# Kernel optimization log

Hardware: AMD Instinct MI355X
Metric: run time of the kernel (lower is better)

The kernel has to match this reference:

```python
import jax, jax.numpy as jnp
import numpy as np

FEAT_STRIDE = 16
SCORE_THRESH = 0.7
DIST_THRESH = 16.0
MAX_OUT = 50
B = 2048
IMG_W = 65536


def setup_inputs() -> dict:
    key = jax.random.key(0)
    k1, k2, k3 = jax.random.split(key, 3)
    fw = IMG_W // FEAT_STRIDE
    pred_cls_logit = jax.random.normal(k1, (B, fw), dtype=jnp.float32)
    pred_delta = jax.random.normal(k2, (B, fw, 2), dtype=jnp.float32)
    # realistic image widths in [0.5, 1.0] * img_width
    real_images_width = jax.random.uniform(k3, (B,), jnp.float32, 0.5, 1.0) * IMG_W
    return {
        "pred_cls_logit": pred_cls_logit,
        "pred_delta": pred_delta,
        "img_width": IMG_W,
        "real_images_width": real_images_width,
    }


def _nms_one(positions, scores):
    # positions: [N, 2], scores: [N]. Greedy 1D NMS, fixed MAX_OUT iterations.
    centers = positions.mean(axis=1)                      # [N]
    alive0 = scores >= SCORE_THRESH                       # score-threshold filter

    def step(alive, _):
        masked = jnp.where(alive, scores, -1e30)
        i = jnp.argmax(masked)                            # highest remaining score
        has = jnp.any(alive)
        f = has.astype(jnp.float32)                       # 1.0 if a box was picked
        p = positions[i] * f
        s = scores[i] * f
        # suppress everything within DIST_THRESH of picked center (incl. itself)
        new_alive = alive & (jnp.abs(centers - centers[i]) > DIST_THRESH)
        return new_alive, (p, s, f)

    _, (P, S, F) = jax.lax.scan(step, alive0, None, length=MAX_OUT)
    # pad_to_fixed_size: append validity flag column, zero-padded rows
    nms_positions = jnp.concatenate([P, F[:, None]], axis=1)   # [MAX_OUT, 3]
    nms_scores = jnp.concatenate([S[:, None], F[:, None]], axis=1)  # [MAX_OUT, 2]
    return nms_positions, nms_scores


def reference(pred_cls_logit, pred_delta, img_width, real_images_width):
    feat_width = img_width // FEAT_STRIDE
    interval_center = (jnp.arange(feat_width, dtype=jnp.float32) + 0.5) * FEAT_STRIDE
    # [B, feat_width, 2]
    pos = pred_delta * FEAT_STRIDE + interval_center[None, :, None]
    scores = jax.nn.sigmoid(pred_cls_logit)               # [B, feat_width]
    max_width = real_images_width[:, None, None] - 1.0
    pos = jnp.where(pos < 0.0, 0.0, pos)
    pos = jnp.where(pos > max_width, max_width, pos)

    nms_positions, nms_scores = jax.vmap(_nms_one)(pos, scores)

    nms_center = nms_positions[..., :2].mean(axis=2)      # [B, MAX_OUT]
    x_interval_num = jnp.floor(nms_center / FEAT_STRIDE).astype(jnp.int32)
    valid = nms_positions[..., 2] == 1.0
    idx = jnp.where(valid, x_interval_num, feat_width)    # out-of-range -> dropped
    cls_ids = jax.vmap(
        lambda ii: jnp.zeros((feat_width,), jnp.float32).at[ii].set(1.0, mode='drop')
    )(idx)                                                # [B, feat_width]
    return nms_positions, nms_scores, cls_ids
```

## Files before the change

kernel.cpp:

```cpp
#include <hip/hip_runtime.h>
#include <math.h>

#define FW 4096
#define MAX_OUT 50
#define WCAP 320
#define NSLOT 1024
#define T0 0.885f
#define T0BITS 0x3F628F5Cu
#define SELCAP 128


__global__ __launch_bounds__(256) void essp_k1(
    const float* __restrict__ logits,
    const float* __restrict__ deltas,
    const float* __restrict__ realw,
    float* stage)
{
  __shared__ float Lx[4][WCAP];
  __shared__ int   Li[4][WCAP];
  __shared__ int   Lcnt[4];
  __shared__ int   Lsel, Lalv;

  const int row  = blockIdx.x;
  const int tid  = threadIdx.x;
  const int lane = tid & 63;
  const int w    = tid >> 6;

  if (tid == 0) { Lsel = 0; Lalv = 0; }

  const float mw = realw[row] - 1.0f;
  const float* lgr = logits + (size_t)row * FW;
  const float* dlr = deltas + (size_t)row * (2 * FW);
  const unsigned long long below = (1ULL << lane) - 1ULL;

  int cnt = 0;
  #pragma unroll
  for (int r = 0; r < 4; ++r) {
    const int i0 = w * 1024 + r * 256 + 4 * lane;
    const float4 lx = *(const float4*)(lgr + i0);
    const float xs[4] = {lx.x, lx.y, lx.z, lx.w};
    bool c4[4]; unsigned long long m4[4];
    #pragma unroll
    for (int e = 0; e < 4; ++e) { c4[e] = (xs[e] >= 0.846f); m4[e] = __ballot(c4[e]); }
    int base = cnt + __popcll(m4[0] & below) + __popcll(m4[1] & below)
                   + __popcll(m4[2] & below) + __popcll(m4[3] & below);
    int off = 0;
    #pragma unroll
    for (int e = 0; e < 4; ++e) {
      if (c4[e]) {
        const int slot = base + off;
        if (slot < WCAP) { Lx[w][slot] = xs[e]; Li[w][slot] = i0 + e; }
        ++off;
      }
    }
    cnt += __popcll(m4[0]) + __popcll(m4[1]) + __popcll(m4[2]) + __popcll(m4[3]);
  }
  if (lane == 0) Lcnt[w] = (cnt < WCAP) ? cnt : WCAP;
  __syncthreads();

  const int c0 = Lcnt[0], c1 = Lcnt[1], c2 = Lcnt[2], c3 = Lcnt[3];
  const int p1 = c0, p2 = c0 + c1, p3 = c0 + c1 + c2;
  int nc = p3 + c3; nc = (nc < NSLOT) ? nc : NSLOT;

  float* Srow = stage + (size_t)row * FW;
  unsigned short* idxrow = (unsigned short*)(Srow + 2048);
  unsigned* keyrow = (unsigned*)(Srow + 2560);

  #pragma unroll
  for (int g0 = 0; g0 < NSLOT; g0 += 256) {
    const int g = g0 + tid;
    float score = -1e30f, cen = 0.0f;
    int idx = 0;
    if (g < nc) {
      const int wsel = (g >= p1) + (g >= p2) + (g >= p3);
      int pre = 0;
      pre = (wsel == 1) ? p1 : pre;
      pre = (wsel == 2) ? p2 : pre;
      pre = (wsel == 3) ? p3 : pre;
      const int kk = g - pre;
      const float x = (&Lx[0][0])[wsel * WCAP + kk];
      idx = (&Li[0][0])[wsel * WCAP + kk];
      const float2 d = *(const float2*)(dlr + 2 * idx);
      const float ic = ((float)idx + 0.5f) * 16.0f;
      float q0 = d.x * 16.0f + ic;
      float q1 = d.y * 16.0f + ic;
      q0 = (q0 < 0.f) ? 0.f : q0;  q0 = (q0 > mw) ? mw : q0;
      q1 = (q1 < 0.f) ? 0.f : q1;  q1 = (q1 > mw) ? mw : q1;
      cen = (q0 + q1) * 0.5f;
      const float s = (float)(1.0 / (1.0 + exp(-(double)x)));
      score = (s >= 0.7f) ? s : -1e30f;
    }
    Srow[g]        = score;
    Srow[1024 + g] = cen;
    idxrow[g]      = (unsigned short)idx;

    const unsigned long long am = __ballot(score >= 0.7f);
    if (lane == 0) atomicAdd(&Lalv, __popcll(am));
    const unsigned long long sm = __ballot(score >= T0);
    int sbase = 0;
    if (lane == 0 && sm) sbase = atomicAdd(&Lsel, __popcll(sm));
    sbase = __shfl(sbase, 0, 64);
    if (score >= T0) {
      const int pos = sbase + __popcll(sm & below);
      if (pos < SELCAP) {
        keyrow[pos] = ((__float_as_uint(score) - T0BITS + 1u) << 10)
                      | (unsigned)(1023 - g);
        Srow[2688 + pos] = cen;
      }
    }
  }
  __syncthreads();
  if (tid == 0) {
    *(int*)(Srow + 2944) = Lsel;
    *(int*)(Srow + 2945) = Lalv;
  }
}

#define KDEF(J, SS, CE)                                                       \
  const unsigned kb##J = ((SS) >= 0.7f) ? __float_as_uint(SS) : 0u;           \
  const float c##J = (CE);

#define INIT1F(J, SLOTEXPR)                                                   \
  unsigned long long fk##J = kb##J                                            \
      ? ((((unsigned long long)kb##J) << 11) | (unsigned)(2047 - (SLOTEXPR))) \
      : 0ULL;

#define M2(RK, RC, KA, CA, KB, CB)                                            \
  const bool t##RK = (KB) > (KA);                                             \
  const unsigned long long RK = t##RK ? (KB) : (KA);                          \
  const float RC = t##RK ? (CB) : (CA);

#define BSTEP(CTRL) {                                                         \
  const unsigned lo_ = (unsigned)__builtin_amdgcn_update_dpp(                 \
      (int)(unsigned)bk, (int)(unsigned)bk, CTRL, 0xF, 0xF, false);           \
  const unsigned hi_ = (unsigned)__builtin_amdgcn_update_dpp(                 \
      (int)(unsigned)(bk >> 32), (int)(unsigned)(bk >> 32), CTRL, 0xF, 0xF,   \
      false);                                                                 \
  const float oc_ = __int_as_float(__builtin_amdgcn_update_dpp(               \
      __float_as_int(bc), __float_as_int(bc), CTRL, 0xF, 0xF, false));        \
  const unsigned long long ok_ = ((unsigned long long)hi_ << 32) | lo_;       \
  const bool tb_ = ok_ > bk;                                                  \
  bk = tb_ ? ok_ : bk;  bc = tb_ ? oc_ : bc; }

#define SUPF(J) {                                                             \
  const bool ts_ = fabsf(c##J - wc) <= 16.0f;                                 \
  fk##J = ts_ ? 0ULL : fk##J; }

struct PR { int pkv; float psv; };

__device__ __attribute__((noinline)) PR heavy_nms(const float* Srow, int lane) {
  const int l4 = 4 * lane;
  const float4 s4a = *(const float4*)(Srow + l4);
  const float4 s4b = *(const float4*)(Srow + 256 + l4);
  const float4 s4c = *(const float4*)(Srow + 512 + l4);
  const float4 s4d = *(const float4*)(Srow + 768 + l4);
  const float4 e4a = *(const float4*)(Srow + 1024 + l4);
  const float4 e4b = *(const float4*)(Srow + 1280 + l4);
  const float4 e4c = *(const float4*)(Srow + 1536 + l4);
  const float4 e4d = *(const float4*)(Srow + 1792 + l4);

  KDEF(0,  s4a.x, e4a.x)  KDEF(1,  s4a.y, e4a.y)
  KDEF(2,  s4a.z, e4a.z)  KDEF(3,  s4a.w, e4a.w)
  KDEF(4,  s4b.x, e4b.x)  KDEF(5,  s4b.y, e4b.y)
  KDEF(6,  s4b.z, e4b.z)  KDEF(7,  s4b.w, e4b.w)
  KDEF(8,  s4c.x, e4c.x)  KDEF(9,  s4c.y, e4c.y)
  KDEF(10, s4c.z, e4c.z)  KDEF(11, s4c.w, e4c.w)
  KDEF(12, s4d.x, e4d.x)  KDEF(13, s4d.y, e4d.y)
  KDEF(14, s4d.z, e4d.z)  KDEF(15, s4d.w, e4d.w)

  INIT1F(0,  l4 + 0)       INIT1F(1,  l4 + 1)       INIT1F(2,  l4 + 2)
  INIT1F(3,  l4 + 3)       INIT1F(4,  256 + l4 + 0) INIT1F(5,  256 + l4 + 1)
  INIT1F(6,  256 + l4 + 2) INIT1F(7,  256 + l4 + 3) INIT1F(8,  512 + l4 + 0)
  INIT1F(9,  512 + l4 + 1) INIT1F(10, 512 + l4 + 2) INIT1F(11, 512 + l4 + 3)
  INIT1F(12, 768 + l4 + 0) INIT1F(13, 768 + l4 + 1) INIT1F(14, 768 + l4 + 2)
  INIT1F(15, 768 + l4 + 3)

  int pkv = -1; float psv = 0.f;
  #pragma unroll 1
  for (int it = 0; it < MAX_OUT; ++it) {
    M2(ka0, ca0, fk0,  c0,  fk1,  c1)
    M2(ka1, ca1, fk2,  c2,  fk3,  c3)
    M2(ka2, ca2, fk4,  c4,  fk5,  c5)
    M2(ka3, ca3, fk6,  c6,  fk7,  c7)
    M2(ka4, ca4, fk8,  c8,  fk9,  c9)
    M2(ka5, ca5, fk10, c10, fk11, c11)
    M2(ka6, ca6, fk12, c12, fk13, c13)
    M2(ka7, ca7, fk14, c14, fk15, c15)
    M2(kb0, cb0, ka0, ca0, ka1, ca1)
    M2(kb1, cb1, ka2, ca2, ka3, ca3)
    M2(kb2, cb2, ka4, ca4, ka5, ca5)
    M2(kb3, cb3, ka6, ca6, ka7, ca7)
    M2(kc0, cc0, kb0, cb0, kb1, cb1)
    M2(kc1, cc1, kb2, cb2, kb3, cb3)
    M2(kd0, cd0, kc0, cc0, kc1, cc1)

    unsigned long long bk = kd0;
    float bc = cd0;
    BSTEP(0xB1) BSTEP(0x4E) BSTEP(0x141) BSTEP(0x140) BSTEP(0x142) BSTEP(0x143)

    const unsigned rhi = (unsigned)__builtin_amdgcn_readlane(
        (int)(unsigned)(bk >> 32), 63);
    const unsigned rlo = (unsigned)__builtin_amdgcn_readlane(
        (int)(unsigned)bk, 63);
    const float rc = __int_as_float(
        __builtin_amdgcn_readlane(__float_as_int(bc), 63));
    const unsigned sbits = (rhi << 21) | (rlo >> 11);
    const bool valid = sbits != 0u;
    const float wc = valid ? rc : 3.0e38f;
    if (lane == it) {
      pkv = valid ? (2047 - (int)(rlo & 0x7FFu)) : -1;
      psv = __uint_as_float(sbits);
    }
    SUPF(0)  SUPF(1)  SUPF(2)  SUPF(3)  SUPF(4)  SUPF(5)  SUPF(6)  SUPF(7)
    SUPF(8)  SUPF(9)  SUPF(10) SUPF(11) SUPF(12) SUPF(13) SUPF(14) SUPF(15)
  }
  PR r; r.pkv = pkv; r.psv = psv; return r;
}

#define SHX1(v)  (unsigned)__builtin_amdgcn_update_dpp((int)(v), (int)(v), 0xB1, 0xF, 0xF, false)
#define SHX2(v)  (unsigned)__builtin_amdgcn_update_dpp((int)(v), (int)(v), 0x4E, 0xF, 0xF, false)
#define SHX4(v)  (unsigned)__builtin_amdgcn_ds_swizzle((int)(v), 0x101F)
#define SHX8(v)  (unsigned)__builtin_amdgcn_ds_swizzle((int)(v), 0x201F)
#define SHX16(v) (unsigned)__builtin_amdgcn_ds_swizzle((int)(v), 0x401F)
#define SHX32(v) (unsigned)__shfl_xor((int)(v), 32, 64)

#define CEX(SH, J, K) {                                                       \
  const unsigned pk0_ = SH(k0), pk1_ = SH(k1);                                \
  const unsigned pc0_ = SH(c0), pc1_ = SH(c1);                                \
  const bool a_  = (lane & (J)) != 0;                                         \
  const bool b0_ = ((K) <= 32) ? ((lane & (K)) != 0) : false;                 \
  const bool b1_ = ((K) <= 32) ? ((lane & (K)) != 0) : ((K) == 64);           \
  const bool x0_ = (a_ != b0_);                                               \
  const bool x1_ = (a_ != b1_);                                               \
  {                                                                           \
    const bool g_ = (k0 > pk0_);                                              \
    const unsigned mx_ = g_ ? k0 : pk0_;                                      \
    const unsigned mn_ = g_ ? pk0_ : k0;                                      \
    const unsigned kn_ = x0_ ? mn_ : mx_;                                     \
    c0 = (kn_ != k0) ? pc0_ : c0;                                             \
    k0 = kn_;                                                                 \
  }                                                                           \
  {                                                                           \
    const bool g_ = (k1 > pk1_);                                              \
    const unsigned mx_ = g_ ? k1 : pk1_;                                      \
    const unsigned mn_ = g_ ? pk1_ : k1;                                      \
    const unsigned kn_ = x1_ ? mn_ : mx_;                                     \
    c1 = (kn_ != k1) ? pc1_ : c1;                                             \
    k1 = kn_;                                                                 \
  }                                                                           \
}

#define CEXP() {                                                              \
  const bool sw_ = (k1 > k0);                                                 \
  const unsigned tk_ = k0, tc_ = c0;                                          \
  k0 = sw_ ? k1 : k0;  c0 = sw_ ? c1 : c0;                                    \
  k1 = sw_ ? tk_ : k1; c1 = sw_ ? tc_ : c1;                                   \
}

__global__ __launch_bounds__(64) void essp_k2(
    const float* __restrict__ deltas,
    const float* __restrict__ realw,
    float* out_pos,
    float* out_scr,
    float* cls_all)
{
  const int row  = blockIdx.x;
  const int lane = threadIdx.x;
  const int l4   = 4 * lane;
  float* Srow = cls_all + (size_t)row * FW;

  const int sel = *(const int*)(Srow + 2944);
  const int alv = *(const int*)(Srow + 2945);

  int pkv = -1;
  float psv = 0.f;
  bool need_heavy = (sel > SELCAP);

  if (!need_heavy) {
    const unsigned* kp = (const unsigned*)(Srow + 2560);
    unsigned k0 = (lane < sel)      ? kp[lane]      : 0u;
    unsigned k1 = (lane + 64 < sel) ? kp[lane + 64] : 0u;
    unsigned c0 = (lane < sel)
        ? __float_as_uint(Srow[2688 + lane]) : 0u;
    unsigned c1 = (lane + 64 < sel)
        ? __float_as_uint(Srow[2688 + 64 + lane]) : 0u;

    CEX(SHX1, 1, 2)
    CEX(SHX2, 2, 4)   CEX(SHX1, 1, 4)
    CEX(SHX4, 4, 8)   CEX(SHX2, 2, 8)   CEX(SHX1, 1, 8)
    CEX(SHX8, 8, 16)  CEX(SHX4, 4, 16)  CEX(SHX2, 2, 16)  CEX(SHX1, 1, 16)
    CEX(SHX16, 16, 32) CEX(SHX8, 8, 32) CEX(SHX4, 4, 32)  CEX(SHX2, 2, 32)
    CEX(SHX1, 1, 32)
    CEX(SHX32, 32, 64) CEX(SHX16, 16, 64) CEX(SHX8, 8, 64) CEX(SHX4, 4, 64)
    CEX(SHX2, 2, 64)  CEX(SHX1, 1, 64)
    CEXP()
    CEX(SHX32, 32, 128) CEX(SHX16, 16, 128) CEX(SHX8, 8, 128)
    CEX(SHX4, 4, 128)  CEX(SHX2, 2, 128)   CEX(SHX1, 1, 128)

    int npick = 0;
    float pcen = 3.0e33f;
    unsigned pkey = 0u;
    #pragma unroll 1
    for (int i = 0; i < sel && npick < MAX_OUT; ++i) {
      const unsigned kiv = (unsigned)__builtin_amdgcn_readlane(
          (int)(i < 64 ? k0 : k1), i & 63);
      const float civ = __uint_as_float((unsigned)__builtin_amdgcn_readlane(
          (int)(i < 64 ? c0 : c1), i & 63));
      const unsigned long long hm = __ballot(fabsf(pcen - civ) <= 16.0f);
      if (hm == 0ULL) {
        if (lane == npick) { pcen = civ; pkey = kiv; }
        ++npick;
      }
    }
    if (npick < MAX_OUT && alv > sel) {
      need_heavy = true;
    } else if (lane < npick) {
      pkv = 1023 - (int)(pkey & 1023u);
      psv = __uint_as_float(((pkey >> 10) - 1u) + T0BITS);
    }
  }

  if (need_heavy) {
    const PR pr = heavy_nms(Srow, lane);
    pkv = pr.pkv; psv = pr.psv;
  }

  float q0 = 0.f, q1 = 0.f;
  int ci = -1;
  if (lane < MAX_OUT && pkv >= 0) {
    const int idx = ((const unsigned short*)(Srow + 2048))[pkv];
    const float2 d = *(const float2*)(deltas + (size_t)row * (2 * FW) + 2 * idx);
    const float mw = realw[row] - 1.0f;
    const float ic = ((float)idx + 0.5f) * 16.0f;
    q0 = d.x * 16.0f + ic;
    q1 = d.y * 16.0f + ic;
    q0 = (q0 < 0.f) ? 0.f : q0;  q0 = (q0 > mw) ? mw : q0;
    q1 = (q1 < 0.f) ? 0.f : q1;  q1 = (q1 > mw) ? mw : q1;
    ci = (int)floorf(((q0 + q1) * 0.5f) * 0.0625f);
  }
  asm volatile("s_waitcnt vmcnt(0)" ::: "memory");

  const float4 z4 = make_float4(0.f, 0.f, 0.f, 0.f);
  #pragma unroll
  for (int q = 0; q < 16; ++q)
    *(float4*)(Srow + 256 * q + l4) = z4;
  asm volatile("s_waitcnt vmcnt(0)" ::: "memory");

  float* prow = out_pos + (size_t)row * (MAX_OUT * 3);
  float* srow = out_scr + (size_t)row * (MAX_OUT * 2);
  if (lane < MAX_OUT) {
    if (pkv >= 0) {
      prow[3 * lane + 0] = q0;
      prow[3 * lane + 1] = q1;
      prow[3 * lane + 2] = 1.0f;
      srow[2 * lane + 0] = psv;
      srow[2 * lane + 1] = 1.0f;
      if (ci >= 0 && ci < FW) Srow[ci] = 1.0f;
    } else {
      prow[3 * lane + 0] = 0.0f;
      prow[3 * lane + 1] = 0.0f;
      prow[3 * lane + 2] = 0.0f;
      srow[2 * lane + 0] = 0.0f;
      srow[2 * lane + 1] = 0.0f;
    }
  }
}

extern "C" void kernel_launch(void* const* d_in, const int* in_sizes, int n_in,
                              void* d_out, int out_size, void* d_ws, size_t ws_size,
                              hipStream_t stream) {
  const float* logits = (const float*)d_in[0];
  const float* deltas = (const float*)d_in[1];
  const float* realw  = (const float*)d_in[3];
  const int Bn = in_sizes[3];
  float* out_pos = (float*)d_out;
  float* out_scr = out_pos + (size_t)Bn * MAX_OUT * 3;
  float* out_cls = out_scr + (size_t)Bn * MAX_OUT * 2;

  essp_k1<<<Bn, 256, 0, stream>>>(logits, deltas, realw, out_cls);
  essp_k2<<<Bn, 64, 0, stream>>>(deltas, realw, out_pos, out_scr, out_cls);
}
```

Baseline: 71.52 us.

## Rewrite k2 NMS as ballot-driven suppression and fuse cls mask into single write

```diff
diff --git a/kernel.cpp b/kernel.cpp
--- a/kernel.cpp
+++ b/kernel.cpp
@@ -257,16 +257,21 @@
   k1 = sw_ ? tk_ : k1; c1 = sw_ ? tc_ : c1;                                   \
 }
 
-__global__ __launch_bounds__(64) void essp_k2(
+__global__ __launch_bounds__(256) void essp_k2(
     const float* __restrict__ deltas,
     const float* __restrict__ realw,
     float* out_pos,
     float* out_scr,
-    float* cls_all)
+    float* cls_all,
+    int Bn)
 {
-  const int row  = blockIdx.x;
-  const int lane = threadIdx.x;
-  const int l4   = 4 * lane;
+  __shared__ unsigned LmLo[4][64];
+  __shared__ unsigned LmHi[4][64];
+
+  const int lane = threadIdx.x & 63;
+  const int w    = threadIdx.x >> 6;
+  const int row  = blockIdx.x * 4 + w;
+  if (row >= Bn) return;
   float* Srow = cls_all + (size_t)row * FW;
 
   const int sel = *(const int*)(Srow + 2944);
@@ -297,21 +302,34 @@
     CEX(SHX32, 32, 128) CEX(SHX16, 16, 128) CEX(SHX8, 8, 128)
     CEX(SHX4, 4, 128)  CEX(SHX2, 2, 128)   CEX(SHX1, 1, 128)
 
+    const float fc0 = __uint_as_float(c0);
+    const float fc1 = __uint_as_float(c1);
+
+    bool a0 = (k0 != 0u), a1 = (k1 != 0u);
     int npick = 0;
-    float pcen = 3.0e33f;
     unsigned pkey = 0u;
     #pragma unroll 1
-    for (int i = 0; i < sel && npick < MAX_OUT; ++i) {
-      const unsigned kiv = (unsigned)__builtin_amdgcn_readlane(
-          (int)(i < 64 ? k0 : k1), i & 63);
-      const float civ = __uint_as_float((unsigned)__builtin_amdgcn_readlane(
-          (int)(i < 64 ? c0 : c1), i & 63));
-      const unsigned long long hm = __ballot(fabsf(pcen - civ) <= 16.0f);
-      if (hm == 0ULL) {
-        if (lane == npick) { pcen = civ; pkey = kiv; }
-        ++npick;
-      }
-    }
+    for (;;) {
+      const unsigned long long m0 = __ballot(a0);
+      const unsigned long long m1 = __ballot(a1);
+      if ((m0 | m1) == 0ULL || npick >= MAX_OUT) break;
+      const int r = (m0 != 0ULL) ? (__ffsll(m0) - 1)
+                                 : (64 + __ffsll(m1) - 1);
+      const int rl = r & 63;
+      const float wa = __int_as_float(
+          __builtin_amdgcn_readlane(__float_as_int(fc0), rl));
+      const float wb = __int_as_float(
+          __builtin_amdgcn_readlane(__float_as_int(fc1), rl));
+      const unsigned kra = (unsigned)__builtin_amdgcn_readlane((int)k0, rl);
+      const unsigned krb = (unsigned)__builtin_amdgcn_readlane((int)k1, rl);
+      const float wc = (r < 64) ? wa : wb;
+      const unsigned kr = (r < 64) ? kra : krb;
+      if (lane == npick) pkey = kr;
+      a0 = a0 && (fabsf(fc0 - wc) > 16.0f);
+      a1 = a1 && (fabsf(fc1 - wc) > 16.0f);
+      ++npick;
+    }
+
     if (npick < MAX_OUT && alv > sel) {
       need_heavy = true;
     } else if (lane < npick) {
@@ -340,11 +358,27 @@
   }
   asm volatile("s_waitcnt vmcnt(0)" ::: "memory");
 
-  const float4 z4 = make_float4(0.f, 0.f, 0.f, 0.f);
+  LmLo[w][lane] = 0u;
+  LmHi[w][lane] = 0u;
+  if (lane < MAX_OUT && pkv >= 0 && ci >= 0 && ci < FW) {
+    const int owner = (ci >> 2) & 63;
+    const int bit = ((ci >> 8) << 2) | (ci & 3);
+    if (bit < 32) atomicOr(&LmLo[w][owner], 1u << bit);
+    else          atomicOr(&LmHi[w][owner], 1u << (bit - 32));
+  }
+  const unsigned mlo = LmLo[w][lane];
+  const unsigned mhi = LmHi[w][lane];
+
   #pragma unroll
-  for (int q = 0; q < 16; ++q)
-    *(float4*)(Srow + 256 * q + l4) = z4;
-  asm volatile("s_waitcnt vmcnt(0)" ::: "memory");
+  for (int q = 0; q < 16; ++q) {
+    const unsigned nib = (q < 8) ? (mlo >> (4 * q)) : (mhi >> (4 * (q - 8)));
+    float4 v;
+    v.x = (nib & 1u) ? 1.0f : 0.0f;
+    v.y = (nib & 2u) ? 1.0f : 0.0f;
+    v.z = (nib & 4u) ? 1.0f : 0.0f;
+    v.w = (nib & 8u) ? 1.0f : 0.0f;
+    *(float4*)(Srow + 256 * q + 4 * lane) = v;
+  }
 
   float* prow = out_pos + (size_t)row * (MAX_OUT * 3);
   float* srow = out_scr + (size_t)row * (MAX_OUT * 2);
@@ -355,7 +389,6 @@
       prow[3 * lane + 2] = 1.0f;
       srow[2 * lane + 0] = psv;
       srow[2 * lane + 1] = 1.0f;
-      if (ci >= 0 && ci < FW) Srow[ci] = 1.0f;
     } else {
       prow[3 * lane + 0] = 0.0f;
       prow[3 * lane + 1] = 0.0f;
@@ -378,5 +411,6 @@
   float* out_cls = out_scr + (size_t)Bn * MAX_OUT * 2;
 
   essp_k1<<<Bn, 256, 0, stream>>>(logits, deltas, realw, out_cls);
-  essp_k2<<<Bn, 64, 0, stream>>>(deltas, realw, out_pos, out_scr, out_cls);
-}
+  essp_k2<<<(Bn + 3) / 4, 256, 0, stream>>>(deltas, realw,
+                                            out_pos, out_scr, out_cls, Bn);
+}
```

New measurement: 70.82 us. About the same (-1.0%).
